# Kernel tuning notes

Measured on AMD Instinct MI355X. Metric: run time of the kernel, lower is better.

Reference implementation:

```python
import jax, jax.numpy as jnp
import numpy as np

N_COLS = 107
CAT_SLICES = [(1, 10), (10, 26), (27, 34), (34, 49), (49, 55), (55, 60), (60, 62), (65, 107)]
MSE_COLS = [0, 26, 62, 63, 64]
BATCH = 524288


def setup_inputs() -> dict:
    key = jax.random.key(0)
    k_dec, k_cont, k_cat = jax.random.split(key, 3)
    data_decoded = jax.random.normal(k_dec, (BATCH, N_COLS), dtype=jnp.float32)
    # Build data_true: continuous cols random, categorical slices exactly one-hot.
    data_true = jax.random.uniform(k_cont, (BATCH, N_COLS), dtype=jnp.float32)
    rows = jnp.arange(BATCH)
    for i, (s, e) in enumerate(CAT_SLICES):
        kk = jax.random.fold_in(k_cat, i)
        labels = jax.random.randint(kk, (BATCH,), 0, e - s)
        data_true = data_true.at[:, s:e].set(0.0)
        data_true = data_true.at[rows, s + labels].set(1.0)
    return {"data_decoded": data_decoded, "data_true": data_true, "batch_size": BATCH}


def _ce(logits, onehot_true):
    # torch nonzero()[:,1] on an exact one-hot slice == argmax
    labels = jnp.argmax(onehot_true, axis=1)
    logp = jax.nn.log_softmax(logits, axis=1)
    return -jnp.mean(jnp.take_along_axis(logp, labels[:, None], axis=1))


def _mse(a, b):
    d = a - b
    return jnp.mean(d * d)


def reference(data_decoded, data_true, batch_size):
    mse_loss = jnp.float32(0.0)
    for c in MSE_COLS:
        mse_loss = mse_loss + _mse(data_decoded[:, c], data_true[:, c])
    ce_loss = jnp.float32(0.0)
    for s, e in CAT_SLICES:
        ce_loss = ce_loss + _ce(data_decoded[:, s:e], data_true[:, s:e])
    multi_loss = mse_loss + ce_loss
    return multi_loss, mse_loss, ce_loss
```

## Files before the change

### kernel.cpp

```cpp
#include <hip/hip_runtime.h>

#define NCOLS 107
#define ROWS_PER_TILE 16
#define TILE_FLOATS (ROWS_PER_TILE * NCOLS)
#define TILE_VEC (TILE_FLOATS / 4)
#define THREADS 256
#define WAVES_PER_BLOCK 4
#define BLOCKS 1280
#define NWAVES (BLOCKS * WAVES_PER_BLOCK)

typedef float f4 __attribute__((ext_vector_type(4)));

template<int S, int E>
__device__ __forceinline__ float slice_lse(const float* dr) {
    constexpr int L = E - S;
    float s = 0.0f;
#pragma unroll
    for (int j = 0; j < L; ++j) s += __expf(dr[S + j]);
    return __logf(s);
}

__device__ __forceinline__ void lin4(int idx, f4 dv, f4 tv, bool valid,
                                     float& mse, float& dot) {
    unsigned c4  = (unsigned)idx * 4u;
    unsigned row = c4 / NCOLS;
    unsigned col = c4 - row * NCOLS;
#pragma unroll
    for (int k = 0; k < 4; ++k) {
        float d = dv[k], tt = tv[k];
        bool ismse = (col == 0) | (col == 26) | ((unsigned)(col - 62) <= 2u);
        float df = d - tt;
        mse += (valid && ismse)  ? df * df : 0.0f;
        dot += (valid && !ismse) ? d * tt  : 0.0f;
        ++col; if (col >= NCOLS) col = 0;
    }
}

__global__ __launch_bounds__(THREADS) void multiloss_main(
        const float* __restrict__ dec, const float* __restrict__ tru,
        float2* __restrict__ ws, int ntiles) {
    __shared__ float sdec[WAVES_PER_BLOCK * TILE_FLOATS];
    int lane  = threadIdx.x & 63;
    float* buf = sdec + (threadIdx.x >> 6) * TILE_FLOATS;
    f4* b4 = (f4*)buf;
    int gwave = (blockIdx.x * THREADS + threadIdx.x) >> 6;

    bool v6 = lane < (TILE_VEC - 384);
    int  i6 = v6 ? (384 + lane) : (TILE_VEC - 1);

    float mse = 0.0f, dot = 0.0f, lse = 0.0f;

    int tile = gwave;
    {
        const f4* gd = (const f4*)dec + (size_t)tile * TILE_VEC;
        const f4* gt = (const f4*)tru + (size_t)tile * TILE_VEC;
        f4 d0 = gd[lane], d1 = gd[64+lane], d2 = gd[128+lane], d3 = gd[192+lane],
           d4 = gd[256+lane], d5 = gd[320+lane], d6 = gd[i6];
        f4 t0 = gt[lane], t1 = gt[64+lane], t2 = gt[128+lane], t3 = gt[192+lane],
           t4 = gt[256+lane], t5 = gt[320+lane], t6 = gt[i6];

        while (tile < ntiles) {
            b4[lane] = d0; b4[64+lane] = d1; b4[128+lane] = d2;
            b4[192+lane] = d3; b4[256+lane] = d4; b4[320+lane] = d5;
            b4[i6] = d6;
            lin4(lane,     d0, t0, true, mse, dot);
            lin4(64+lane,  d1, t1, true, mse, dot);
            lin4(128+lane, d2, t2, true, mse, dot);
            lin4(192+lane, d3, t3, true, mse, dot);
            lin4(256+lane, d4, t4, true, mse, dot);
            lin4(320+lane, d5, t5, true, mse, dot);
            lin4(i6,       d6, t6, v6,   mse, dot);
            int nt = tile + NWAVES;
            if (nt < ntiles) {
                const f4* ngd = (const f4*)dec + (size_t)nt * TILE_VEC;
                const f4* ngt = (const f4*)tru + (size_t)nt * TILE_VEC;
                d0 = ngd[lane]; d1 = ngd[64+lane]; d2 = ngd[128+lane];
                d3 = ngd[192+lane]; d4 = ngd[256+lane]; d5 = ngd[320+lane];
                d6 = ngd[i6];
                t0 = ngt[lane]; t1 = ngt[64+lane]; t2 = ngt[128+lane];
                t3 = ngt[192+lane]; t4 = ngt[256+lane]; t5 = ngt[320+lane];
                t6 = ngt[i6];
            }
            int row  = lane & 15;
            int part = lane >> 4;
            const float* dr = buf + row * NCOLS;
            if (part == 0) {
                lse += slice_lse<65, 107>(dr);
            } else if (part == 1) {
                lse += slice_lse<10, 26>(dr) + slice_lse<34, 49>(dr);
            } else if (part == 2) {
                lse += slice_lse<1, 10>(dr) + slice_lse<27, 34>(dr)
                     + slice_lse<49, 55>(dr);
            } else {
                lse += slice_lse<55, 60>(dr) + slice_lse<60, 62>(dr);
            }
            tile = nt;
        }
    }

    float ce = lse - dot;
#pragma unroll
    for (int off = 32; off > 0; off >>= 1) {
        mse += __shfl_down(mse, off, 64);
        ce  += __shfl_down(ce,  off, 64);
    }
    if (lane == 0)
        ws[gwave] = make_float2(mse, ce);
}

__global__ __launch_bounds__(256) void multiloss_fin(
        const float2* __restrict__ ws, float* __restrict__ out,
        int nslots, float invN) {
    float m = 0.0f, c = 0.0f;
    for (int i = threadIdx.x; i < nslots; i += 256) {
        float2 v = ws[i];
        m += v.x; c += v.y;
    }
#pragma unroll
    for (int off = 32; off > 0; off >>= 1) {
        m += __shfl_down(m, off, 64);
        c += __shfl_down(c, off, 64);
    }
    __shared__ float sm[4], sc[4];
    int wid  = threadIdx.x >> 6;
    int lane = threadIdx.x & 63;
    if (lane == 0) { sm[wid] = m; sc[wid] = c; }
    __syncthreads();
    if (threadIdx.x == 0) {
        float mse = (sm[0] + sm[1] + sm[2] + sm[3]) * invN;
        float ce  = (sc[0] + sc[1] + sc[2] + sc[3]) * invN;
        out[0] = mse + ce;
        out[1] = mse;
        out[2] = ce;
    }
}

extern "C" void kernel_launch(void* const* d_in, const int* in_sizes, int n_in,
                              void* d_out, int out_size, void* d_ws, size_t ws_size,
                              hipStream_t stream) {
    const float* dec = (const float*)d_in[0];
    const float* tru = (const float*)d_in[1];
    int nrows  = in_sizes[0] / NCOLS;
    int ntiles = nrows / ROWS_PER_TILE;
    float2* ws = (float2*)d_ws;
    multiloss_main<<<BLOCKS, THREADS, 0, stream>>>(dec, tru, ws, ntiles);
    multiloss_fin<<<1, 256, 0, stream>>>(ws, (float*)d_out, NWAVES,
                                         1.0f / (float)nrows);
}
```

Before: 440.5 us.

## Assign four whole rows per thread and drop the shared-memory staging

Each thread now processes a group of 4 rows (107 float4s) straight from global memory. A compile-time template walk routes every element either to MSE or to the running per-slice exp sums, and the log of each slice's sum is taken at its last column. The LDS staging, grid-stride loop and register prefetch are gone, and the grid grows to one thread per group. In exchange, each thread's loads are strided by 1712 bytes, so coalescing across a wavefront is poor, and register pressure rises sharply. More waves also go through the final reduction.

```diff
diff --git a/kernel.cpp b/kernel.cpp
--- a/kernel.cpp
+++ b/kernel.cpp
@@ -1,109 +1,80 @@
 #include <hip/hip_runtime.h>
 
 #define NCOLS 107
-#define ROWS_PER_TILE 16
-#define TILE_FLOATS (ROWS_PER_TILE * NCOLS)
-#define TILE_VEC (TILE_FLOATS / 4)
+#define ROWS_PER_GROUP 4
+#define GROUP_F4 NCOLS
 #define THREADS 256
-#define WAVES_PER_BLOCK 4
-#define BLOCKS 1280
-#define NWAVES (BLOCKS * WAVES_PER_BLOCK)
 
 typedef float f4 __attribute__((ext_vector_type(4)));
 
-template<int S, int E>
-__device__ __forceinline__ float slice_lse(const float* dr) {
-    constexpr int L = E - S;
-    float s = 0.0f;
-#pragma unroll
-    for (int j = 0; j < L; ++j) s += __expf(dr[S + j]);
-    return __logf(s);
+__device__ __host__ __forceinline__ constexpr int slice_of(int col) {
+    return (col >= 1  && col < 10) ? 0 :
+           (col >= 10 && col < 26) ? 1 :
+           (col >= 27 && col < 34) ? 2 :
+           (col >= 34 && col < 49) ? 3 :
+           (col >= 49 && col < 55) ? 4 :
+           (col >= 55 && col < 60) ? 5 :
+           (col >= 60 && col < 62) ? 6 :
+           (col >= 65)             ? 7 : -1;
+}
+__device__ __host__ __forceinline__ constexpr int slice_last(int sid) {
+    return sid == 0 ?  9 : sid == 1 ? 25 : sid == 2 ? 33 : sid == 3 ? 48 :
+           sid == 4 ? 54 : sid == 5 ? 59 : sid == 6 ? 61 : 106;
 }
 
-__device__ __forceinline__ void lin4(int idx, f4 dv, f4 tv, bool valid,
-                                     float& mse, float& dot) {
-    unsigned c4  = (unsigned)idx * 4u;
-    unsigned row = c4 / NCOLS;
-    unsigned col = c4 - row * NCOLS;
-#pragma unroll
-    for (int k = 0; k < 4; ++k) {
-        float d = dv[k], tt = tv[k];
-        bool ismse = (col == 0) | (col == 26) | ((unsigned)(col - 62) <= 2u);
-        float df = d - tt;
-        mse += (valid && ismse)  ? df * df : 0.0f;
-        dot += (valid && !ismse) ? d * tt  : 0.0f;
-        ++col; if (col >= NCOLS) col = 0;
+template<int L>
+__device__ __forceinline__ void elem(float d, float t, float (&s)[8],
+                                     float& mse, float& dot, float& lse) {
+    constexpr int col = L % NCOLS;
+    constexpr int sid = slice_of(col);
+    if constexpr (sid < 0) {
+        float df = d - t;
+        mse += df * df;
+    } else {
+        s[sid] += __expf(d);
+        dot = __builtin_fmaf(d, t, dot);
+        if constexpr (col == slice_last(sid)) {
+            lse += __logf(s[sid]);
+            s[sid] = 0.0f;
+        }
     }
 }
 
-__global__ __launch_bounds__(THREADS) void multiloss_main(
+template<int C>
+__device__ __forceinline__ void walk(const f4* __restrict__ gd,
+                                     const f4* __restrict__ gt,
+                                     float (&s)[8],
+                                     float& mse, float& dot, float& lse) {
+    if constexpr (C < GROUP_F4) {
+        f4 dv = gd[C];
+        f4 tv = gt[C];
+        elem<4 * C + 0>(dv[0], tv[0], s, mse, dot, lse);
+        elem<4 * C + 1>(dv[1], tv[1], s, mse, dot, lse);
+        elem<4 * C + 2>(dv[2], tv[2], s, mse, dot, lse);
+        elem<4 * C + 3>(dv[3], tv[3], s, mse, dot, lse);
+        walk<C + 1>(gd, gt, s, mse, dot, lse);
+    }
+}
+
+__global__ __launch_bounds__(THREADS, 2) void multiloss_main(
         const float* __restrict__ dec, const float* __restrict__ tru,
-        float2* __restrict__ ws, int ntiles) {
-    __shared__ float sdec[WAVES_PER_BLOCK * TILE_FLOATS];
-    int lane  = threadIdx.x & 63;
-    float* buf = sdec + (threadIdx.x >> 6) * TILE_FLOATS;
-    f4* b4 = (f4*)buf;
-    int gwave = (blockIdx.x * THREADS + threadIdx.x) >> 6;
-
-    bool v6 = lane < (TILE_VEC - 384);
-    int  i6 = v6 ? (384 + lane) : (TILE_VEC - 1);
-
+        float2* __restrict__ ws, int ngroups) {
+    int g = blockIdx.x * THREADS + threadIdx.x;
     float mse = 0.0f, dot = 0.0f, lse = 0.0f;
-
-    int tile = gwave;
-    {
-        const f4* gd = (const f4*)dec + (size_t)tile * TILE_VEC;
-        const f4* gt = (const f4*)tru + (size_t)tile * TILE_VEC;
-        f4 d0 = gd[lane], d1 = gd[64+lane], d2 = gd[128+lane], d3 = gd[192+lane],
-           d4 = gd[256+lane], d5 = gd[320+lane], d6 = gd[i6];
-        f4 t0 = gt[lane], t1 = gt[64+lane], t2 = gt[128+lane], t3 = gt[192+lane],
-           t4 = gt[256+lane], t5 = gt[320+lane], t6 = gt[i6];
-
-        while (tile < ntiles) {
-            b4[lane] = d0; b4[64+lane] = d1; b4[128+lane] = d2;
-            b4[192+lane] = d3; b4[256+lane] = d4; b4[320+lane] = d5;
-            b4[i6] = d6;
-            lin4(lane,     d0, t0, true, mse, dot);
-            lin4(64+lane,  d1, t1, true, mse, dot);
-            lin4(128+lane, d2, t2, true, mse, dot);
-            lin4(192+lane, d3, t3, true, mse, dot);
-            lin4(256+lane, d4, t4, true, mse, dot);
-            lin4(320+lane, d5, t5, true, mse, dot);
-            lin4(i6,       d6, t6, v6,   mse, dot);
-            int nt = tile + NWAVES;
-            if (nt < ntiles) {
-                const f4* ngd = (const f4*)dec + (size_t)nt * TILE_VEC;
-                const f4* ngt = (const f4*)tru + (size_t)nt * TILE_VEC;
-                d0 = ngd[lane]; d1 = ngd[64+lane]; d2 = ngd[128+lane];
-                d3 = ngd[192+lane]; d4 = ngd[256+lane]; d5 = ngd[320+lane];
-                d6 = ngd[i6];
-                t0 = ngt[lane]; t1 = ngt[64+lane]; t2 = ngt[128+lane];
-                t3 = ngt[192+lane]; t4 = ngt[256+lane]; t5 = ngt[320+lane];
-                t6 = ngt[i6];
-            }
-            int row  = lane & 15;
-            int part = lane >> 4;
-            const float* dr = buf + row * NCOLS;
-            if (part == 0) {
-                lse += slice_lse<65, 107>(dr);
-            } else if (part == 1) {
-                lse += slice_lse<10, 26>(dr) + slice_lse<34, 49>(dr);
-            } else if (part == 2) {
-                lse += slice_lse<1, 10>(dr) + slice_lse<27, 34>(dr)
-                     + slice_lse<49, 55>(dr);
-            } else {
-                lse += slice_lse<55, 60>(dr) + slice_lse<60, 62>(dr);
-            }
-            tile = nt;
-        }
+    float s[8] = {0.0f, 0.0f, 0.0f, 0.0f, 0.0f, 0.0f, 0.0f, 0.0f};
+    if (g < ngroups) {
+        const f4* gd = (const f4*)dec + (size_t)g * GROUP_F4;
+        const f4* gt = (const f4*)tru + (size_t)g * GROUP_F4;
+        walk<0>(gd, gt, s, mse, dot, lse);
     }
-
     float ce = lse - dot;
 #pragma unroll
     for (int off = 32; off > 0; off >>= 1) {
         mse += __shfl_down(mse, off, 64);
         ce  += __shfl_down(ce,  off, 64);
     }
+    int lane  = threadIdx.x & 63;
+    int gwave = (blockIdx.x * THREADS + threadIdx.x) >> 6;
     if (lane == 0)
         ws[gwave] = make_float2(mse, ce);
 }
@@ -140,10 +111,12 @@
                               hipStream_t stream) {
     const float* dec = (const float*)d_in[0];
     const float* tru = (const float*)d_in[1];
-    int nrows  = in_sizes[0] / NCOLS;
-    int ntiles = nrows / ROWS_PER_TILE;
+    int nrows   = in_sizes[0] / NCOLS;
+    int ngroups = nrows / ROWS_PER_GROUP;
+    int nblocks = (ngroups + THREADS - 1) / THREADS;
+    int nwaves  = nblocks * (THREADS / 64);
     float2* ws = (float2*)d_ws;
-    multiloss_main<<<BLOCKS, THREADS, 0, stream>>>(dec, tru, ws, ntiles);
-    multiloss_fin<<<1, 256, 0, stream>>>(ws, (float*)d_out, NWAVES,
+    multiloss_main<<<nblocks, THREADS, 0, stream>>>(dec, tru, ws, ngroups);
+    multiloss_fin<<<1, 256, 0, stream>>>(ws, (float*)d_out, nwaves,
                                          1.0f / (float)nrows);
 }
```

New measurement: 520.1 us. 1.18x slower.
